# Kernel optimization log

Measured on AMD Instinct MI355X. Metric: run time of the kernel, lower is better.

## Reference

```python
import jax, jax.numpy as jnp
import numpy as np

VX, VY = 0.2, 0.2
X_OFF = VX / 2 + 0.0          # vx/2 + pc_range[0]
Y_OFF = VY / 2 + (-40.0)      # vy/2 + pc_range[1]
K = 8                          # hardcoded in GCNLayer
BN_EPS = 1e-3
LRELU_SLOPE = 0.2
V, T, C_IN, C_OUT = 4096, 100, 4, 64


def _gcn_layer(x, conv_w, bn_gamma, bn_beta, bn_mean, bn_var):
    """DGCNN EdgeConv layer. x: [N, T, C]. Returns [N, T, O]."""
    N, Tn, C = x.shape
    # KNN on negative squared distance (self included in topk, as in torch code)
    xx = jnp.sum(x * x, axis=-1)                       # [N, T]
    inner = jnp.einsum('ntc,nsc->nts', x, x)           # [N, T, T]
    neg_dist = 2.0 * inner - xx[:, :, None] - xx[:, None, :]
    _, idx = jax.lax.top_k(neg_dist, K)                # [N, T, K]
    # gather neighbor features: nbr[n,t,k,c] = x[n, idx[n,t,k], c]
    nbr = x[jnp.arange(N)[:, None, None], idx]         # [N, T, K, C]
    xc = x[:, :, None, :]                              # [N, T, 1, C]
    edge = jnp.concatenate(
        [nbr - xc, jnp.broadcast_to(xc, (N, Tn, K, C))], axis=-1)  # [N,T,K,2C]
    # 1x1 conv (no bias) + eval-mode BatchNorm + LeakyReLU(0.2)
    h = jnp.einsum('ntkc,oc->ntko', edge, conv_w)      # [N, T, K, O]
    scale = bn_gamma / jnp.sqrt(bn_var + BN_EPS)
    h = (h - bn_mean) * scale + bn_beta
    h = jax.nn.leaky_relu(h, LRELU_SLOPE)
    return jnp.max(h, axis=2)                          # max over k -> [N, T, O]


def setup_inputs() -> dict:
    key = jax.random.key(0)
    k1, k2, k3, k4, k5, k6 = jax.random.split(key, 6)
    features = jax.random.normal(k1, (V, T, C_IN), dtype=jnp.float32)
    num_voxels = jnp.maximum(
        jax.random.randint(k2, (V,), 0, T), 1).astype(jnp.int32)
    coors = jax.random.randint(k3, (V, 4), 0, 352).astype(jnp.int32)
    # GCNLayer params: Conv2d(18, 64, 1, bias=False) + BatchNorm2d(64)
    conv_w = jax.random.normal(k4, (C_OUT, 18), dtype=jnp.float32) * 0.1
    bn_gamma = jnp.ones((C_OUT,), jnp.float32)
    bn_beta = jnp.zeros((C_OUT,), jnp.float32)
    bn_mean = jax.random.normal(k5, (C_OUT,), jnp.float32) * 0.1
    bn_var = 1.0 + 0.1 * jax.random.uniform(k6, (C_OUT,), jnp.float32)
    return {"features": features, "conv_w": conv_w, "bn_gamma": bn_gamma,
            "bn_beta": bn_beta, "bn_mean": bn_mean, "bn_var": bn_var,
            "num_voxels": num_voxels, "coors": coors}


def reference(features, conv_w, bn_gamma, bn_beta, bn_mean, bn_var,
              num_voxels, coors):
    nv = num_voxels.astype(features.dtype)
    # decorate: cluster offsets (xyz - mean) and pillar-center offsets (xy)
    points_mean = jnp.sum(features[:, :, :3], axis=1, keepdims=True) / nv[:, None, None]
    f_cluster = features[:, :, :3] - points_mean                      # [V,T,3]
    fx = features[:, :, 0] - (coors[:, 3].astype(features.dtype)[:, None] * VX + X_OFF)
    fy = features[:, :, 1] - (coors[:, 2].astype(features.dtype)[:, None] * VY + Y_OFF)
    f_center = jnp.stack([fx, fy], axis=-1)                           # [V,T,2]
    feat = jnp.concatenate([features, f_cluster, f_center], axis=-1)  # [V,T,9]
    # padding mask: point t valid iff t < num_voxels[v]
    mask = (jnp.arange(T)[None, :] < num_voxels[:, None]).astype(features.dtype)
    feat = feat * mask[:, :, None]
    # single GCN (last) layer; batch_process chunking is a no-op mathematically
    out = _gcn_layer(feat, conv_w, bn_gamma, bn_beta, bn_mean, bn_var)  # [V,T,64]
    out = out * mask[:, :, None]            # (+ zeros prev_features_out)
    out = jnp.max(out, axis=1)              # max over points -> [V, 64]
    return out
```

## Files before the change

kernel.cpp:

```cpp
#include <hip/hip_runtime.h>

#define TPTS 100
#define CO   64
#define KK   8
#define NW   8

__device__ __forceinline__ unsigned umin_(unsigned a, unsigned b) { return a < b ? a : b; }
__device__ __forceinline__ _Float16 hmax_(_Float16 a, _Float16 b) { return a > b ? a : b; }

__device__ __forceinline__ unsigned med3u(unsigned a, unsigned b, unsigned c) {
    unsigned d;
    asm("v_med3_u32 %0, %1, %2, %3" : "=v"(d) : "v"(a), "v"(b), "v"(c));
    return d;
}

__device__ __forceinline__ unsigned dist_key(const float4 qt, const float4 qs, unsigned s) {
    float dx = qt.x - qs.x, dy = qt.y - qs.y;
    float dz = qt.z - qs.z, dw = qt.w - qs.w;
    float e = __fmaf_rn(dx, dx, __fmaf_rn(dy, dy, __fmaf_rn(dz, dz, dw * dw)));
    return (__float_as_uint(e) & 0xFFFFFF80u) | s;
}

__device__ __forceinline__ void ins8(unsigned val[KK], unsigned key) {
    #pragma unroll
    for (int k = KK - 1; k >= 1; --k)
        val[k] = med3u(val[k - 1], val[k], key);
    val[0] = umin_(val[0], key);
}

__global__ __launch_bounds__(512) void dgcnn_kernel(
    const float* __restrict__ features,
    const float* __restrict__ conv_w,
    const float* __restrict__ bn_gamma,
    const float* __restrict__ bn_beta,
    const float* __restrict__ bn_mean,
    const float* __restrict__ bn_var,
    const int*  __restrict__ num_voxels,
    const int*  __restrict__ coors,
    float* __restrict__ out)
{
    __shared__ float    s_q[TPTS][4];
    __shared__ float    s_xx[TPTS];
    __shared__ unsigned s_idxp[TPTS][2];
    __shared__ float    s_mean[4];
    __shared__ union {
        float    stage[TPTS][4];
        _Float16 g16[TPTS][CO];
        float    red[NW][CO];
    } s_u;

    const float INF = __builtin_inff();
    const int v   = blockIdx.x;
    const int tid = threadIdx.x;
    const int nv  = num_voxels[v];

    float4 f = make_float4(0.f, 0.f, 0.f, 0.f);
    if (tid < TPTS) {
        f = reinterpret_cast<const float4*>(features)[v * TPTS + tid];
        *reinterpret_cast<float4*>(&s_u.stage[tid][0]) = f;
    }
    __syncthreads();

    if (tid < 96) {
        int ch = tid >> 5, j = tid & 31;
        float p = s_u.stage[j][ch] + s_u.stage[j + 32][ch] + s_u.stage[j + 64][ch];
        if (j < 4) p += s_u.stage[j + 96][ch];
        #pragma unroll
        for (int off = 16; off >= 1; off >>= 1)
            p += __shfl_xor(p, off, 32);
        if (j == 0) s_mean[ch] = p / (float)nv;
    }
    __syncthreads();

    const float cx = (float)coors[v * 4 + 3] * 0.2f + 0.1f;
    const float cy = (float)coors[v * 4 + 2] * 0.2f - 39.9f;
    const float m0 = s_mean[0], m1 = s_mean[1], m2 = s_mean[2];

    if (tid < TPTS) {
        float mask = (tid < nv) ? 1.0f : 0.0f;
        float r0 = f.x * mask, r1 = f.y * mask, r2 = f.z * mask, r3 = f.w * mask;
        float r4 = (f.x - m0) * mask;
        float r5 = (f.y - m1) * mask;
        float r6 = (f.z - m2) * mask;
        float r7 = (f.x - cx) * mask;
        float r8 = (f.y - cy) * mask;
        float xx = r0*r0 + r1*r1 + r2*r2 + r3*r3 + r4*r4
                 + r5*r5 + r6*r6 + r7*r7 + r8*r8;
        *reinterpret_cast<float4*>(&s_q[tid][0]) =
            make_float4(1.7320508075688772f * r0,
                        1.7320508075688772f * r1,
                        1.4142135623730951f * r2, r3);
        s_xx[tid] = xx;
    }

    const int o  = tid & 63;
    const int wv = tid >> 6;
    const float sgn = (bn_gamma[o] < 0.f) ? -1.f : 1.f;
    float w1r[9], w2r[9];
    #pragma unroll
    for (int c = 0; c < 9; ++c) {
        float a = conv_w[o * 18 + c];
        float b = conv_w[o * 18 + 9 + c];
        w1r[c] = a * sgn;
        w2r[c] = (b - a) * sgn;
    }
    const float i3 = 0.57735026918962576f, i2 = 0.70710678118654752f;
    float wq1[4], wq2[4];
    wq1[0] = (w1r[0] + w1r[4] + w1r[7]) * i3;
    wq1[1] = (w1r[1] + w1r[5] + w1r[8]) * i3;
    wq1[2] = (w1r[2] + w1r[6]) * i2;
    wq1[3] = w1r[3];
    wq2[0] = (w2r[0] + w2r[4] + w2r[7]) * i3;
    wq2[1] = (w2r[1] + w2r[5] + w2r[8]) * i3;
    wq2[2] = (w2r[2] + w2r[6]) * i2;
    wq2[3] = w2r[3];
    const float c1v = -(w1r[4]*m0 + w1r[5]*m1 + w1r[6]*m2 + w1r[7]*cx + w1r[8]*cy);
    const float c2v = -(w2r[4]*m0 + w2r[5]*m1 + w2r[6]*m2 + w2r[7]*cx + w2r[8]*cy);
    __syncthreads();

    const int nd = (nv + 31) >> 5;

    {
        int r0 = nv + wv;
        if (r0 < TPTS) s_u.g16[r0][o] = (_Float16)0.f;
    }

    if (wv < nd) {
        const int trow = wv * 32 + (o & 31);
        const int bsd  = o >> 5;
        if (trow < nv) {
            const float4 qt = *reinterpret_cast<const float4*>(&s_q[trow][0]);
            unsigned val[KK];
            #pragma unroll
            for (int k = 0; k < KK; ++k) val[k] = 0xFFFFFFFFu;
            int mcnt = TPTS - nv; if (mcnt > KK) mcnt = KK;
            int ha = (nv + mcnt + 1) >> 1; if (ha > nv) ha = nv;
            int s        = bsd ? ha : 0;
            const int se = bsd ? nv : ha;
            #pragma unroll 2
            for (; s < se; ++s) {
                const float4 qs = *reinterpret_cast<const float4*>(&s_q[s][0]);
                ins8(val, dist_key(qt, qs, (unsigned)s));
            }
            if (bsd) {
                unsigned kmb = __float_as_uint(s_xx[trow]) & 0xFFFFFF80u;
                for (int j = 0; j < mcnt; ++j)
                    ins8(val, kmb | (unsigned)(nv + j));
            }
            unsigned other[KK];
            #pragma unroll
            for (int k = 0; k < KK; ++k) other[k] = __shfl_xor(val[k], 32);
            if (!bsd) {
                unsigned m[KK];
                #pragma unroll
                for (int k = 0; k < KK; ++k)
                    m[k] = umin_(val[k], other[KK - 1 - k]) & 127u;
                unsigned p0 = m[0] | (m[1] << 8) | (m[2] << 16) | (m[3] << 24);
                unsigned p1 = m[4] | (m[5] << 8) | (m[6] << 16) | (m[7] << 24);
                *reinterpret_cast<uint2*>(&s_idxp[trow][0]) = make_uint2(p0, p1);
            }
        }
    } else {
        const int step = NW - nd;
        for (int sR = wv - nd; sR < nv; sR += step) {
            const float4 q = *reinterpret_cast<const float4*>(&s_q[sR][0]);
            float g = c1v;
            g = __fmaf_rn(q.x, wq1[0], g);
            g = __fmaf_rn(q.y, wq1[1], g);
            g = __fmaf_rn(q.z, wq1[2], g);
            g = __fmaf_rn(q.w, wq1[3], g);
            s_u.g16[sR][o] = (_Float16)g;
        }
    }
    __syncthreads();

    float acc = -INF;
    for (int tt = wv; tt < nv; tt += NW) {
        const float4 q = *reinterpret_cast<const float4*>(&s_q[tt][0]);
        float base = c2v;
        base = __fmaf_rn(q.x, wq2[0], base);
        base = __fmaf_rn(q.y, wq2[1], base);
        base = __fmaf_rn(q.z, wq2[2], base);
        base = __fmaf_rn(q.w, wq2[3], base);
        uint2 pk = *reinterpret_cast<const uint2*>(&s_idxp[tt][0]);
        int i0 =  pk.x        & 255, i1 = (pk.x >>  8) & 255;
        int i2 = (pk.x >> 16) & 255, i3_ = (pk.x >> 24) & 255;
        int i4 =  pk.y        & 255, i5 = (pk.y >>  8) & 255;
        int i6 = (pk.y >> 16) & 255, i7 = (pk.y >> 24) & 255;
        _Float16 g0 = s_u.g16[i0][o], g1 = s_u.g16[i1][o];
        _Float16 g2 = s_u.g16[i2][o], g3 = s_u.g16[i3_][o];
        _Float16 g4 = s_u.g16[i4][o], g5 = s_u.g16[i5][o];
        _Float16 g6 = s_u.g16[i6][o], g7 = s_u.g16[i7][o];
        _Float16 gm = hmax_(hmax_(hmax_(g0, g1), hmax_(g2, g3)),
                            hmax_(hmax_(g4, g5), hmax_(g6, g7)));
        acc = fmaxf(acc, (float)gm + base);
    }
    __syncthreads();
    s_u.red[wv][o] = acc;
    __syncthreads();

    if (tid < CO) {
        float m = s_u.red[0][tid];
        #pragma unroll
        for (int i = 1; i < NW; ++i) m = fmaxf(m, s_u.red[i][tid]);
        float scale = bn_gamma[tid] / sqrtf(bn_var[tid] + 0.001f);
        float bias  = bn_beta[tid] - bn_mean[tid] * scale;
        float h = m * fabsf(scale) + bias;
        float a = (h > 0.f) ? h : 0.2f * h;
        if (nv < TPTS) a = fmaxf(a, 0.f);
        out[v * CO + tid] = a;
    }
}

extern "C" void kernel_launch(void* const* d_in, const int* in_sizes, int n_in,
                              void* d_out, int out_size, void* d_ws, size_t ws_size,
                              hipStream_t stream) {
    const float* features = (const float*)d_in[0];
    const float* conv_w   = (const float*)d_in[1];
    const float* bn_gamma = (const float*)d_in[2];
    const float* bn_beta  = (const float*)d_in[3];
    const float* bn_mean  = (const float*)d_in[4];
    const float* bn_var   = (const float*)d_in[5];
    const int*   num_vox  = (const int*)d_in[6];
    const int*   coor     = (const int*)d_in[7];
    float* outp = (float*)d_out;
    const int V = in_sizes[6];
    dgcnn_kernel<<<V, 512, 0, stream>>>(features, conv_w, bn_gamma, bn_beta,
                                        bn_mean, bn_var, num_vox, coor, outp);
}
```

Baseline: 108.0 us.

## Split KNN candidate scan across 4-8 lanes per row with shuffle merge

Reworks the KNN top-8 search so each query row is handled by 4 lanes (more than 64 valid points) or 8 lanes (64 or fewer), with every wave taking part. Partial top-8 lists are combined through xor-shuffle bitonic merges. This replaces the old scheme, where some waves scanned rows with 2 lanes each while the remaining waves computed the g table. The aim is to shorten the serial insertion loop and balance work across waves. In exchange it adds shuffle and sort overhead, predicated dummy iterations, and a g-table loop that now runs after KNN in every wave. The conv weights are also loaded as float2 pairs.

```diff
diff --git a/kernel.cpp b/kernel.cpp
--- a/kernel.cpp
+++ b/kernel.cpp
@@ -6,6 +6,7 @@
 #define NW   8
 
 __device__ __forceinline__ unsigned umin_(unsigned a, unsigned b) { return a < b ? a : b; }
+__device__ __forceinline__ unsigned umax_(unsigned a, unsigned b) { return a > b ? a : b; }
 __device__ __forceinline__ _Float16 hmax_(_Float16 a, _Float16 b) { return a > b ? a : b; }
 
 __device__ __forceinline__ unsigned med3u(unsigned a, unsigned b, unsigned c) {
@@ -14,18 +15,44 @@
     return d;
 }
 
-__device__ __forceinline__ unsigned dist_key(const float4 qt, const float4 qs, unsigned s) {
-    float dx = qt.x - qs.x, dy = qt.y - qs.y;
-    float dz = qt.z - qs.z, dw = qt.w - qs.w;
-    float e = __fmaf_rn(dx, dx, __fmaf_rn(dy, dy, __fmaf_rn(dz, dz, dw * dw)));
-    return (__float_as_uint(e) & 0xFFFFFF80u) | s;
-}
-
 __device__ __forceinline__ void ins8(unsigned val[KK], unsigned key) {
     #pragma unroll
     for (int k = KK - 1; k >= 1; --k)
         val[k] = med3u(val[k - 1], val[k], key);
     val[0] = umin_(val[0], key);
+}
+
+__device__ __forceinline__ void hclean(unsigned val[KK], int mask) {
+    unsigned other[KK];
+    #pragma unroll
+    for (int k = 0; k < KK; ++k) other[k] = __shfl_xor(val[k], mask, 64);
+    unsigned t[KK];
+    #pragma unroll
+    for (int k = 0; k < KK; ++k) t[k] = umin_(val[k], other[KK - 1 - k]);
+    #pragma unroll
+    for (int k = 0; k < KK; ++k) val[k] = t[k];
+}
+
+__device__ __forceinline__ void bsort8(unsigned v[KK]) {
+    #pragma unroll
+    for (int k = 0; k < 4; ++k) {
+        unsigned lo = umin_(v[k], v[k + 4]), hi = umax_(v[k], v[k + 4]);
+        v[k] = lo; v[k + 4] = hi;
+    }
+    {
+        unsigned lo, hi;
+        lo = umin_(v[0], v[2]); hi = umax_(v[0], v[2]); v[0] = lo; v[2] = hi;
+        lo = umin_(v[1], v[3]); hi = umax_(v[1], v[3]); v[1] = lo; v[3] = hi;
+        lo = umin_(v[4], v[6]); hi = umax_(v[4], v[6]); v[4] = lo; v[6] = hi;
+        lo = umin_(v[5], v[7]); hi = umax_(v[5], v[7]); v[5] = lo; v[7] = hi;
+    }
+    {
+        unsigned lo, hi;
+        lo = umin_(v[0], v[1]); hi = umax_(v[0], v[1]); v[0] = lo; v[1] = hi;
+        lo = umin_(v[2], v[3]); hi = umax_(v[2], v[3]); v[2] = lo; v[3] = hi;
+        lo = umin_(v[4], v[5]); hi = umax_(v[4], v[5]); v[4] = lo; v[5] = hi;
+        lo = umin_(v[6], v[7]); hi = umax_(v[6], v[7]); v[6] = lo; v[7] = hi;
+    }
 }
 
 __global__ __launch_bounds__(512) void dgcnn_kernel(
@@ -97,12 +124,19 @@
     const int wv = tid >> 6;
     const float sgn = (bn_gamma[o] < 0.f) ? -1.f : 1.f;
     float w1r[9], w2r[9];
-    #pragma unroll
-    for (int c = 0; c < 9; ++c) {
-        float a = conv_w[o * 18 + c];
-        float b = conv_w[o * 18 + 9 + c];
-        w1r[c] = a * sgn;
-        w2r[c] = (b - a) * sgn;
+    {
+        const float2* wrow = reinterpret_cast<const float2*>(conv_w + o * 18);
+        float wa[18];
+        #pragma unroll
+        for (int c = 0; c < 9; ++c) {
+            float2 p = wrow[c];
+            wa[2 * c] = p.x; wa[2 * c + 1] = p.y;
+        }
+        #pragma unroll
+        for (int c = 0; c < 9; ++c) {
+            w1r[c] = wa[c] * sgn;
+            w2r[c] = (wa[9 + c] - wa[c]) * sgn;
+        }
     }
     const float i3 = 0.57735026918962576f, i2 = 0.70710678118654752f;
     float wq1[4], wq2[4];
@@ -118,59 +152,71 @@
     const float c2v = -(w2r[4]*m0 + w2r[5]*m1 + w2r[6]*m2 + w2r[7]*cx + w2r[8]*cy);
     __syncthreads();
 
-    const int nd = (nv + 31) >> 5;
-
     {
         int r0 = nv + wv;
         if (r0 < TPTS) s_u.g16[r0][o] = (_Float16)0.f;
     }
 
-    if (wv < nd) {
-        const int trow = wv * 32 + (o & 31);
-        const int bsd  = o >> 5;
-        if (trow < nv) {
-            const float4 qt = *reinterpret_cast<const float4*>(&s_q[trow][0]);
-            unsigned val[KK];
-            #pragma unroll
-            for (int k = 0; k < KK; ++k) val[k] = 0xFFFFFFFFu;
-            int mcnt = TPTS - nv; if (mcnt > KK) mcnt = KK;
-            int ha = (nv + mcnt + 1) >> 1; if (ha > nv) ha = nv;
-            int s        = bsd ? ha : 0;
-            const int se = bsd ? nv : ha;
-            #pragma unroll 2
-            for (; s < se; ++s) {
-                const float4 qs = *reinterpret_cast<const float4*>(&s_q[s][0]);
-                ins8(val, dist_key(qt, qs, (unsigned)s));
-            }
-            if (bsd) {
-                unsigned kmb = __float_as_uint(s_xx[trow]) & 0xFFFFFF80u;
-                for (int j = 0; j < mcnt; ++j)
-                    ins8(val, kmb | (unsigned)(nv + j));
-            }
-            unsigned other[KK];
-            #pragma unroll
-            for (int k = 0; k < KK; ++k) other[k] = __shfl_xor(val[k], 32);
-            if (!bsd) {
-                unsigned m[KK];
-                #pragma unroll
-                for (int k = 0; k < KK; ++k)
-                    m[k] = umin_(val[k], other[KK - 1 - k]) & 127u;
-                unsigned p0 = m[0] | (m[1] << 8) | (m[2] << 16) | (m[3] << 24);
-                unsigned p1 = m[4] | (m[5] << 8) | (m[6] << 16) | (m[7] << 24);
-                *reinterpret_cast<uint2*>(&s_idxp[trow][0]) = make_uint2(p0, p1);
-            }
-        }
-    } else {
-        const int step = NW - nd;
-        for (int sR = wv - nd; sR < nv; sR += step) {
-            const float4 q = *reinterpret_cast<const float4*>(&s_q[sR][0]);
-            float g = c1v;
-            g = __fmaf_rn(q.x, wq1[0], g);
-            g = __fmaf_rn(q.y, wq1[1], g);
-            g = __fmaf_rn(q.z, wq1[2], g);
-            g = __fmaf_rn(q.w, wq1[3], g);
-            s_u.g16[sR][o] = (_Float16)g;
-        }
+    {
+        const bool big = (nv > 64);
+        const int lr   = big ? (o & 15) : (o & 7);
+        const int sg   = big ? (o >> 4) : (o >> 3);
+        const int trow = wv + 8 * lr;
+        const int tre  = (trow < nv) ? trow : (nv - 1);
+        int mcnt = TPTS - nv; if (mcnt > KK) mcnt = KK;
+        const int L  = nv + mcnt;
+        const int LS = big ? 2 : 3;
+        const int q_ = L >> LS, r_ = L - (q_ << LS);
+        const int len    = q_ + (sg < r_ ? 1 : 0);
+        const int s0     = sg * q_ + (sg < r_ ? sg : r_);
+        const int lenmax = q_ + (r_ ? 1 : 0);
+
+        const float4 qt = *reinterpret_cast<const float4*>(&s_q[tre][0]);
+        const unsigned kmb = __float_as_uint(s_xx[tre]) & 0xFFFFFF80u;
+        unsigned val[KK];
+        #pragma unroll
+        for (int k = 0; k < KK; ++k) val[k] = 0xFFFFFFFFu;
+
+        #pragma unroll 2
+        for (int j = 0; j < lenmax; ++j) {
+            int s  = s0 + j;
+            int sc = (s < TPTS - 1) ? s : (TPTS - 1);
+            const float4 qs = *reinterpret_cast<const float4*>(&s_q[sc][0]);
+            float dx = qt.x - qs.x, dy = qt.y - qs.y;
+            float dz = qt.z - qs.z, dw = qt.w - qs.w;
+            float e = __fmaf_rn(dx, dx, __fmaf_rn(dy, dy,
+                      __fmaf_rn(dz, dz, dw * dw)));
+            unsigned hi = (s < nv) ? (__float_as_uint(e) & 0xFFFFFF80u) : kmb;
+            unsigned key = hi | (unsigned)s;
+            key = (j < len) ? key : 0xFFFFFFFFu;
+            ins8(val, key);
+        }
+
+        if (big) {
+            hclean(val, 16); bsort8(val);
+            hclean(val, 32);
+        } else {
+            hclean(val, 8);  bsort8(val);
+            hclean(val, 16); bsort8(val);
+            hclean(val, 32);
+        }
+        if (sg == 0 && trow < nv) {
+            unsigned p0 =  (val[0] & 127u)        | ((val[1] & 127u) << 8)
+                        | ((val[2] & 127u) << 16) | ((val[3] & 127u) << 24);
+            unsigned p1 =  (val[4] & 127u)        | ((val[5] & 127u) << 8)
+                        | ((val[6] & 127u) << 16) | ((val[7] & 127u) << 24);
+            *reinterpret_cast<uint2*>(&s_idxp[trow][0]) = make_uint2(p0, p1);
+        }
+    }
+
+    for (int sR = wv; sR < nv; sR += NW) {
+        const float4 q = *reinterpret_cast<const float4*>(&s_q[sR][0]);
+        float g = c1v;
+        g = __fmaf_rn(q.x, wq1[0], g);
+        g = __fmaf_rn(q.y, wq1[1], g);
+        g = __fmaf_rn(q.z, wq1[2], g);
+        g = __fmaf_rn(q.w, wq1[3], g);
+        s_u.g16[sR][o] = (_Float16)g;
     }
     __syncthreads();
 
@@ -184,13 +230,13 @@
         base = __fmaf_rn(q.w, wq2[3], base);
         uint2 pk = *reinterpret_cast<const uint2*>(&s_idxp[tt][0]);
         int i0 =  pk.x        & 255, i1 = (pk.x >>  8) & 255;
-        int i2 = (pk.x >> 16) & 255, i3_ = (pk.x >> 24) & 255;
+        int i2_ = (pk.x >> 16) & 255, i3_ = (pk.x >> 24) & 255;
         int i4 =  pk.y        & 255, i5 = (pk.y >>  8) & 255;
         int i6 = (pk.y >> 16) & 255, i7 = (pk.y >> 24) & 255;
-        _Float16 g0 = s_u.g16[i0][o], g1 = s_u.g16[i1][o];
-        _Float16 g2 = s_u.g16[i2][o], g3 = s_u.g16[i3_][o];
-        _Float16 g4 = s_u.g16[i4][o], g5 = s_u.g16[i5][o];
-        _Float16 g6 = s_u.g16[i6][o], g7 = s_u.g16[i7][o];
+        _Float16 g0 = s_u.g16[i0][o],  g1 = s_u.g16[i1][o];
+        _Float16 g2 = s_u.g16[i2_][o], g3 = s_u.g16[i3_][o];
+        _Float16 g4 = s_u.g16[i4][o],  g5 = s_u.g16[i5][o];
+        _Float16 g6 = s_u.g16[i6][o],  g7 = s_u.g16[i7][o];
         _Float16 gm = hmax_(hmax_(hmax_(g0, g1), hmax_(g2, g3)),
                             hmax_(hmax_(g4, g5), hmax_(g6, g7)));
         acc = fmaxf(acc, (float)gm + base);
```

After: 114.1 us. +5.6%, slower.

## Pack two fp16 channels per lane and use packed max in gather stage

Applied to the files above, without the earlier changes.

Each lane now handles two adjacent output channels, written and read as packed fp16 pairs, with v_pk_max_f16 for the neighbor max. Each wave covers two points per iteration, so the number of LDS gather loads per channel pair is halved. The weights for the paired channels are exchanged with shuffles. The reduction buffer moves out of the union so the trailing barrier can be dropped, and the conv weight loads are vectorized as float2. The cost is extra shuffles, more registers, and duplicated FMA work per lane.

```diff
diff --git a/kernel.cpp b/kernel.cpp
--- a/kernel.cpp
+++ b/kernel.cpp
@@ -6,7 +6,6 @@
 #define NW   8
 
 __device__ __forceinline__ unsigned umin_(unsigned a, unsigned b) { return a < b ? a : b; }
-__device__ __forceinline__ _Float16 hmax_(_Float16 a, _Float16 b) { return a > b ? a : b; }
 
 __device__ __forceinline__ unsigned med3u(unsigned a, unsigned b, unsigned c) {
     unsigned d;
@@ -14,11 +13,10 @@
     return d;
 }
 
-__device__ __forceinline__ unsigned dist_key(const float4 qt, const float4 qs, unsigned s) {
-    float dx = qt.x - qs.x, dy = qt.y - qs.y;
-    float dz = qt.z - qs.z, dw = qt.w - qs.w;
-    float e = __fmaf_rn(dx, dx, __fmaf_rn(dy, dy, __fmaf_rn(dz, dz, dw * dw)));
-    return (__float_as_uint(e) & 0xFFFFFF80u) | s;
+__device__ __forceinline__ unsigned pkmaxh(unsigned a, unsigned b) {
+    unsigned d;
+    asm("v_pk_max_f16 %0, %1, %2" : "=v"(d) : "v"(a), "v"(b));
+    return d;
 }
 
 __device__ __forceinline__ void ins8(unsigned val[KK], unsigned key) {
@@ -42,11 +40,11 @@
     __shared__ float    s_q[TPTS][4];
     __shared__ float    s_xx[TPTS];
     __shared__ unsigned s_idxp[TPTS][2];
+    __shared__ float    s_red[NW][CO];
     __shared__ float    s_mean[4];
     __shared__ union {
         float    stage[TPTS][4];
         _Float16 g16[TPTS][CO];
-        float    red[NW][CO];
     } s_u;
 
     const float INF = __builtin_inff();
@@ -93,16 +91,25 @@
         s_xx[tid] = xx;
     }
 
-    const int o  = tid & 63;
-    const int wv = tid >> 6;
+    const int o   = tid & 63;
+    const int wv  = tid >> 6;
+    const int o2  = o & 31;
+    const int hlf = o >> 5;
     const float sgn = (bn_gamma[o] < 0.f) ? -1.f : 1.f;
     float w1r[9], w2r[9];
-    #pragma unroll
-    for (int c = 0; c < 9; ++c) {
-        float a = conv_w[o * 18 + c];
-        float b = conv_w[o * 18 + 9 + c];
-        w1r[c] = a * sgn;
-        w2r[c] = (b - a) * sgn;
+    {
+        const float2* wrow = reinterpret_cast<const float2*>(conv_w + o * 18);
+        float wa[18];
+        #pragma unroll
+        for (int c = 0; c < 9; ++c) {
+            float2 p = wrow[c];
+            wa[2 * c] = p.x; wa[2 * c + 1] = p.y;
+        }
+        #pragma unroll
+        for (int c = 0; c < 9; ++c) {
+            w1r[c] = wa[c] * sgn;
+            w2r[c] = (wa[9 + c] - wa[c]) * sgn;
+        }
     }
     const float i3 = 0.57735026918962576f, i2 = 0.70710678118654752f;
     float wq1[4], wq2[4];
@@ -116,6 +123,17 @@
     wq2[3] = w2r[3];
     const float c1v = -(w1r[4]*m0 + w1r[5]*m1 + w1r[6]*m2 + w1r[7]*cx + w1r[8]*cy);
     const float c2v = -(w2r[4]*m0 + w2r[5]*m1 + w2r[6]*m2 + w2r[7]*cx + w2r[8]*cy);
+
+    float wq1A[4], wq1B[4], wq2A[4], wq2B[4];
+    #pragma unroll
+    for (int c = 0; c < 4; ++c) {
+        wq1A[c] = __shfl(wq1[c], 2 * o2);
+        wq1B[c] = __shfl(wq1[c], 2 * o2 + 1);
+        wq2A[c] = __shfl(wq2[c], 2 * o2);
+        wq2B[c] = __shfl(wq2[c], 2 * o2 + 1);
+    }
+    const float c1A = __shfl(c1v, 2 * o2), c1B = __shfl(c1v, 2 * o2 + 1);
+    const float c2A = __shfl(c2v, 2 * o2), c2B = __shfl(c2v, 2 * o2 + 1);
     __syncthreads();
 
     const int nd = (nv + 31) >> 5;
@@ -140,7 +158,11 @@
             #pragma unroll 2
             for (; s < se; ++s) {
                 const float4 qs = *reinterpret_cast<const float4*>(&s_q[s][0]);
-                ins8(val, dist_key(qt, qs, (unsigned)s));
+                float dx = qt.x - qs.x, dy = qt.y - qs.y;
+                float dz = qt.z - qs.z, dw = qt.w - qs.w;
+                float e = __fmaf_rn(dx, dx, __fmaf_rn(dy, dy,
+                          __fmaf_rn(dz, dz, dw * dw)));
+                ins8(val, (__float_as_uint(e) & 0xFFFFFF80u) | (unsigned)s);
             }
             if (bsd) {
                 unsigned kmb = __float_as_uint(s_xx[trow]) & 0xFFFFFF80u;
@@ -161,48 +183,72 @@
             }
         }
     } else {
-        const int step = NW - nd;
-        for (int sR = wv - nd; sR < nv; sR += step) {
-            const float4 q = *reinterpret_cast<const float4*>(&s_q[sR][0]);
-            float g = c1v;
-            g = __fmaf_rn(q.x, wq1[0], g);
-            g = __fmaf_rn(q.y, wq1[1], g);
-            g = __fmaf_rn(q.z, wq1[2], g);
-            g = __fmaf_rn(q.w, wq1[3], g);
-            s_u.g16[sR][o] = (_Float16)g;
-        }
-    }
-    __syncthreads();
-
-    float acc = -INF;
-    for (int tt = wv; tt < nv; tt += NW) {
-        const float4 q = *reinterpret_cast<const float4*>(&s_q[tt][0]);
-        float base = c2v;
-        base = __fmaf_rn(q.x, wq2[0], base);
-        base = __fmaf_rn(q.y, wq2[1], base);
-        base = __fmaf_rn(q.z, wq2[2], base);
-        base = __fmaf_rn(q.w, wq2[3], base);
-        uint2 pk = *reinterpret_cast<const uint2*>(&s_idxp[tt][0]);
+        const int nE = NW - nd;
+        for (int r = (wv - nd) * 2 + hlf; r < nv; r += 2 * nE) {
+            const float4 q = *reinterpret_cast<const float4*>(&s_q[r][0]);
+            float gA = c1A;
+            gA = __fmaf_rn(q.x, wq1A[0], gA);
+            gA = __fmaf_rn(q.y, wq1A[1], gA);
+            gA = __fmaf_rn(q.z, wq1A[2], gA);
+            gA = __fmaf_rn(q.w, wq1A[3], gA);
+            float gB = c1B;
+            gB = __fmaf_rn(q.x, wq1B[0], gB);
+            gB = __fmaf_rn(q.y, wq1B[1], gB);
+            gB = __fmaf_rn(q.z, wq1B[2], gB);
+            gB = __fmaf_rn(q.w, wq1B[3], gB);
+            _Float16 hA = (_Float16)gA, hB = (_Float16)gB;
+            unsigned pk = ((unsigned)__builtin_bit_cast(unsigned short, hB) << 16)
+                        |  (unsigned)__builtin_bit_cast(unsigned short, hA);
+            *reinterpret_cast<unsigned*>(&s_u.g16[r][2 * o2]) = pk;
+        }
+    }
+    __syncthreads();
+
+    float accA = -INF, accB = -INF;
+    for (int t = wv * 2 + hlf; t < nv; t += 16) {
+        const float4 q = *reinterpret_cast<const float4*>(&s_q[t][0]);
+        float baseA = c2A;
+        baseA = __fmaf_rn(q.x, wq2A[0], baseA);
+        baseA = __fmaf_rn(q.y, wq2A[1], baseA);
+        baseA = __fmaf_rn(q.z, wq2A[2], baseA);
+        baseA = __fmaf_rn(q.w, wq2A[3], baseA);
+        float baseB = c2B;
+        baseB = __fmaf_rn(q.x, wq2B[0], baseB);
+        baseB = __fmaf_rn(q.y, wq2B[1], baseB);
+        baseB = __fmaf_rn(q.z, wq2B[2], baseB);
+        baseB = __fmaf_rn(q.w, wq2B[3], baseB);
+        uint2 pk = *reinterpret_cast<const uint2*>(&s_idxp[t][0]);
         int i0 =  pk.x        & 255, i1 = (pk.x >>  8) & 255;
-        int i2 = (pk.x >> 16) & 255, i3_ = (pk.x >> 24) & 255;
+        int i2_ = (pk.x >> 16) & 255, i3_ = (pk.x >> 24) & 255;
         int i4 =  pk.y        & 255, i5 = (pk.y >>  8) & 255;
         int i6 = (pk.y >> 16) & 255, i7 = (pk.y >> 24) & 255;
-        _Float16 g0 = s_u.g16[i0][o], g1 = s_u.g16[i1][o];
-        _Float16 g2 = s_u.g16[i2][o], g3 = s_u.g16[i3_][o];
-        _Float16 g4 = s_u.g16[i4][o], g5 = s_u.g16[i5][o];
-        _Float16 g6 = s_u.g16[i6][o], g7 = s_u.g16[i7][o];
-        _Float16 gm = hmax_(hmax_(hmax_(g0, g1), hmax_(g2, g3)),
-                            hmax_(hmax_(g4, g5), hmax_(g6, g7)));
-        acc = fmaxf(acc, (float)gm + base);
-    }
-    __syncthreads();
-    s_u.red[wv][o] = acc;
+        unsigned g0 = *reinterpret_cast<const unsigned*>(&s_u.g16[i0][2 * o2]);
+        unsigned g1 = *reinterpret_cast<const unsigned*>(&s_u.g16[i1][2 * o2]);
+        unsigned g2 = *reinterpret_cast<const unsigned*>(&s_u.g16[i2_][2 * o2]);
+        unsigned g3 = *reinterpret_cast<const unsigned*>(&s_u.g16[i3_][2 * o2]);
+        unsigned g4 = *reinterpret_cast<const unsigned*>(&s_u.g16[i4][2 * o2]);
+        unsigned g5 = *reinterpret_cast<const unsigned*>(&s_u.g16[i5][2 * o2]);
+        unsigned g6 = *reinterpret_cast<const unsigned*>(&s_u.g16[i6][2 * o2]);
+        unsigned g7 = *reinterpret_cast<const unsigned*>(&s_u.g16[i7][2 * o2]);
+        unsigned gm = pkmaxh(pkmaxh(pkmaxh(g0, g1), pkmaxh(g2, g3)),
+                             pkmaxh(pkmaxh(g4, g5), pkmaxh(g6, g7)));
+        float gA = (float)__builtin_bit_cast(_Float16, (unsigned short)(gm & 0xFFFFu));
+        float gB = (float)__builtin_bit_cast(_Float16, (unsigned short)(gm >> 16));
+        accA = fmaxf(accA, gA + baseA);
+        accB = fmaxf(accB, gB + baseB);
+    }
+    accA = fmaxf(accA, __shfl_xor(accA, 32));
+    accB = fmaxf(accB, __shfl_xor(accB, 32));
+    if (hlf == 0) {
+        s_red[wv][2 * o2]     = accA;
+        s_red[wv][2 * o2 + 1] = accB;
+    }
     __syncthreads();
 
     if (tid < CO) {
-        float m = s_u.red[0][tid];
-        #pragma unroll
-        for (int i = 1; i < NW; ++i) m = fmaxf(m, s_u.red[i][tid]);
+        float m = s_red[0][tid];
+        #pragma unroll
+        for (int i = 1; i < NW; ++i) m = fmaxf(m, s_red[i][tid]);
         float scale = bn_gamma[tid] / sqrtf(bn_var[tid] + 0.001f);
         float bias  = bn_beta[tid] - bn_mean[tid] * scale;
         float h = m * fabsf(scale) + bias;
```

Measured after the change: 105.9 us. About the same (-1.9%).
